# Kernel tuning notes

Hardware: AMD Instinct MI355X
Metric: run time of the kernel (lower is better)

## Reference

```python
import jax, jax.numpy as jnp
import numpy as np

EMBED = 1024
NUM_EXPERTS = 8
TOP_K = 2


def setup_inputs() -> dict:
    key = jax.random.key(0)
    ks = jax.random.split(key, 6)
    scale = EMBED ** -0.5  # keep activations numerically sane
    return {
        "x": jax.random.normal(ks[0], (4, 4096, EMBED), jnp.float32),
        "router_w": jax.random.normal(ks[1], (EMBED, NUM_EXPERTS), jnp.float32) * scale,
        "router_b": jnp.zeros((NUM_EXPERTS,), jnp.float32),
        "we_gate": jax.random.normal(ks[2], (NUM_EXPERTS, EMBED, EMBED), jnp.float32) * scale,
        "we_up": jax.random.normal(ks[3], (NUM_EXPERTS, EMBED, EMBED), jnp.float32) * scale,
        "we_down": jax.random.normal(ks[4], (NUM_EXPERTS, EMBED, EMBED), jnp.float32) * scale,
    }


def reference(x, router_w, router_b, we_gate, we_up, we_down):
    x_shape = x.shape
    x_flat = x.reshape(-1, x_shape[-1])            # [T, D]
    num_tokens = x_flat.shape[0]

    router_logits = x_flat @ router_w + router_b    # [T, E]
    topk_weights, topk_indices = jax.lax.top_k(router_logits, k=TOP_K)
    topk_weights = jax.nn.softmax(topk_weights, axis=-1)  # [T, K]

    token_idx_mesh = jnp.repeat(jnp.arange(num_tokens), TOP_K)  # [T*K]
    expert_idx_mesh = topk_indices.reshape(-1)                  # [T*K]

    sort_permutation = jnp.argsort(expert_idx_mesh)  # stable sort by expert
    sorted_expert_idx = expert_idx_mesh[sort_permutation]
    sorted_token_idx = token_idx_mesh[sort_permutation]
    group_sizes = jnp.bincount(sorted_expert_idx, length=NUM_EXPERTS)

    sorted_tokens = x_flat[sorted_token_idx]  # [T*K, D] gather (ragged dispatch)

    ff_gate = jax.lax.ragged_dot(sorted_tokens, we_gate, group_sizes)  # [T*K, D]
    ff_up = jax.lax.ragged_dot(sorted_tokens, we_up, group_sizes)      # [T*K, D]
    activated = jax.nn.silu(ff_gate) * ff_up
    ff_out = jax.lax.ragged_dot(activated, we_down, group_sizes)       # [T*K, D]

    # fuse router weighting into the combine (scatter-add) step
    sorted_weights = topk_weights.reshape(-1)[sort_permutation]  # [T*K]
    ff_out = ff_out * sorted_weights[:, None]

    output_flat = jnp.zeros_like(x_flat).at[sorted_token_idx].add(ff_out)
    return output_flat.reshape(x_shape)
```

## Files before the change

### kernel.cpp

```cpp
#include <hip/hip_runtime.h>
#include <hip/hip_bf16.h>
#include <cstdint>
#include <cstddef>

typedef unsigned short u16;
typedef unsigned int u32;
typedef __attribute__((ext_vector_type(8))) short short8;
typedef __attribute__((ext_vector_type(4))) float floatx4;

#define DD 1024
#define NE 8

#define GLOAD_LDS16(G, L)                                               \
  __builtin_amdgcn_global_load_lds(                                     \
      (const __attribute__((address_space(1))) void*)(G),               \
      (__attribute__((address_space(3))) void*)(L), 16, 0, 0)

__device__ __forceinline__ u16 f2bf(float f) {
  union { __hip_bfloat16 h; u16 u; } cv;
  cv.h = __float2bfloat16(f);
  return cv.u;
}

__device__ __forceinline__ float2 bf2f2(u32 u) {
  union { u32 v; float f; } lo, hi;
  lo.v = u << 16; hi.v = u & 0xffff0000u;
  float2 r; r.x = lo.f; r.y = hi.f; return r;
}

__global__ __launch_bounds__(256) void router_kernel(
    const float* __restrict__ x, const float* __restrict__ rw,
    const float* __restrict__ rb, int2* __restrict__ experts,
    float2* __restrict__ wts, u16* __restrict__ xbf, int T) {
  const int wave = threadIdx.x >> 6;
  const int lane = threadIdx.x & 63;
  const int t = blockIdx.x * 4 + wave;
  if (t >= T) return;
  const float* xr = x + (size_t)t * DD;
  float acc[NE] = {0.f, 0.f, 0.f, 0.f, 0.f, 0.f, 0.f, 0.f};
#pragma unroll
  for (int i = 0; i < 16; i++) {
    const int idx = lane + i * 64;
    const float xv = xr[idx];
    xbf[(size_t)t * DD + idx] = f2bf(xv);
    const float4* r4 = (const float4*)(rw + (size_t)idx * NE);
    float4 a = r4[0], b = r4[1];
    acc[0] += xv * a.x; acc[1] += xv * a.y; acc[2] += xv * a.z; acc[3] += xv * a.w;
    acc[4] += xv * b.x; acc[5] += xv * b.y; acc[6] += xv * b.z; acc[7] += xv * b.w;
  }
#pragma unroll
  for (int s = 1; s < 64; s <<= 1)
#pragma unroll
    for (int e = 0; e < NE; e++)
      acc[e] += __shfl_xor(acc[e], s);
  if (lane == 0) {
    float lg[NE];
#pragma unroll
    for (int e = 0; e < NE; e++) lg[e] = acc[e] + rb[e];
    float l0 = lg[0]; int i0 = 0;
#pragma unroll
    for (int e = 1; e < NE; e++) if (lg[e] > l0) { l0 = lg[e]; i0 = e; }
    float l1 = -3.4e38f; int i1 = 0;
#pragma unroll
    for (int e = 0; e < NE; e++) {
      if (e == i0) continue;
      if (lg[e] > l1) { l1 = lg[e]; i1 = e; }
    }
    const float w0 = 1.f / (1.f + expf(l1 - l0));
    experts[t] = make_int2(i0, i1);
    wts[t] = make_float2(w0, 1.f - w0);
  }
}

__global__ __launch_bounds__(256) void count_kernel(
    const int2* __restrict__ experts, int* __restrict__ counts, int T) {
  __shared__ int lc[NE];
  if (threadIdx.x < NE) lc[threadIdx.x] = 0;
  __syncthreads();
  const int t = blockIdx.x * 256 + threadIdx.x;
  if (t < T) {
    int2 e = experts[t];
    atomicAdd(&lc[e.x], 1);
    atomicAdd(&lc[e.y], 1);
  }
  __syncthreads();
  if (threadIdx.x < NE && lc[threadIdx.x] > 0)
    atomicAdd(&counts[threadIdx.x], lc[threadIdx.x]);
}

__global__ void offsets_kernel(const int* __restrict__ counts, int* __restrict__ offsets) {
  int s = 0;
  for (int e = 0; e < NE; e++) { offsets[e] = s; s += counts[e]; }
}

__global__ __launch_bounds__(256) void scatter_kernel(
    const int2* __restrict__ experts, const int* __restrict__ offsets,
    int* __restrict__ cursors, int* __restrict__ tok_id,
    int2* __restrict__ slots, int T) {
  __shared__ int lc[NE], lb[NE];
  if (threadIdx.x < NE) lc[threadIdx.x] = 0;
  __syncthreads();
  const int t = blockIdx.x * 256 + threadIdx.x;
  int2 e = make_int2(0, 0);
  int p0 = 0, p1 = 0;
  if (t < T) {
    e = experts[t];
    p0 = atomicAdd(&lc[e.x], 1);
    p1 = atomicAdd(&lc[e.y], 1);
  }
  __syncthreads();
  if (threadIdx.x < NE) lb[threadIdx.x] = atomicAdd(&cursors[threadIdx.x], lc[threadIdx.x]);
  __syncthreads();
  if (t < T) {
    const int s0 = offsets[e.x] + lb[e.x] + p0;
    const int s1 = offsets[e.y] + lb[e.y] + p1;
    tok_id[s0] = t;
    tok_id[s1] = t;
    slots[t] = make_int2(s0, s1);
  }
}

__global__ __launch_bounds__(256) void convert_kernel(
    const float* __restrict__ wg, const float* __restrict__ wu,
    const float* __restrict__ wd, u16* __restrict__ Wgu, u16* __restrict__ Wd) {
  const int z = blockIdx.z;
  const int mat = z >> 3;
  const int e = z & 7;
  const float* src = (mat == 0 ? wg : (mat == 1 ? wu : wd)) + (size_t)e * DD * DD;
  __shared__ float tile[64][65];
  const int k0 = blockIdx.y * 64, n0 = blockIdx.x * 64;
  const int tx = threadIdx.x & 63, ty = threadIdx.x >> 6;
#pragma unroll
  for (int i = 0; i < 16; i++) {
    const int kk = i * 4 + ty;
    tile[kk][tx] = src[(size_t)(k0 + kk) * DD + n0 + tx];
  }
  __syncthreads();
#pragma unroll
  for (int i = 0; i < 16; i++) {
    const int nn = i * 4 + ty;
    const int n = n0 + nn;
    const u16 h = f2bf(tile[tx][nn]);
    if (mat == 2) {
      Wd[((size_t)e * DD + n) * DD + k0 + tx] = h;
    } else {
      const int nc = ((n >> 3) << 4) | (mat << 3) | (n & 7);
      Wgu[((size_t)e * 2048 + nc) * DD + k0 + tx] = h;
    }
  }
}

__global__ __launch_bounds__(256) void gateup_kernel(
    const u16* __restrict__ xbf, const u16* __restrict__ Wgu,
    const int* __restrict__ tok_id, const int* __restrict__ offsets,
    const int* __restrict__ counts, u16* __restrict__ H) {
  const int e = blockIdx.z;
  const int cnt = counts[e];
  const int m0 = blockIdx.y * 128;
  if (m0 >= cnt) return;
  const int off = offsets[e];
  const int n0 = blockIdx.x * 128;

  __shared__ u16 As[128 * 64];
  __shared__ u16 Bs[128 * 64];

  const int t = threadIdx.x;
  const int lane = t & 63;
  const int wave = t >> 6;
  const int wm = (wave >> 1) * 64;
  const int wn = (wave & 1) * 64;
  const int r16 = lane & 15;
  const int quad = lane >> 4;

  const int drow = t >> 3;
  const int dpos = t & 7;
  const u16* srcA[4];
  const u16* srcB[4];
  const u16* bbase = Wgu + ((size_t)e * 2048 + n0) * DD;
#pragma unroll
  for (int i = 0; i < 4; i++) {
    const int row = drow + i * 32;
    int r = m0 + row; if (r > cnt - 1) r = cnt - 1;
    const int tok = tok_id[off + r];
    const int ka = (dpos ^ (row & 7)) * 8;
    srcA[i] = xbf + (size_t)tok * DD + ka;
    srcB[i] = bbase + (size_t)row * DD + ka;
  }

  floatx4 acc[4][4];
#pragma unroll
  for (int i = 0; i < 4; i++)
#pragma unroll
    for (int j = 0; j < 4; j++)
      acc[i][j] = (floatx4){0.f, 0.f, 0.f, 0.f};

#pragma unroll 1
  for (int k0 = 0; k0 < DD; k0 += 64) {
    __syncthreads();
#pragma unroll
    for (int i = 0; i < 4; i++) {
      GLOAD_LDS16(srcA[i] + k0, &As[t * 8 + i * 2048]);
      GLOAD_LDS16(srcB[i] + k0, &Bs[t * 8 + i * 2048]);
    }
    __syncthreads();
#pragma unroll
    for (int s = 0; s < 2; s++) {
      short8 a[4], b[4];
#pragma unroll
      for (int i = 0; i < 4; i++)
        a[i] = *(const short8*)&As[(wm + i * 16 + r16) * 64 + (((s << 2) + quad) ^ (r16 & 7)) * 8];
#pragma unroll
      for (int j = 0; j < 4; j++)
        b[j] = *(const short8*)&Bs[(wn + j * 16 + r16) * 64 + (((s << 2) + quad) ^ (r16 & 7)) * 8];
#pragma unroll
      for (int i = 0; i < 4; i++)
#pragma unroll
        for (int j = 0; j < 4; j++)
          acc[i][j] = __builtin_amdgcn_mfma_f32_16x16x32_bf16(a[i], b[j], acc[i][j], 0, 0, 0);
    }
  }

#pragma unroll
  for (int i = 0; i < 4; i++) {
    const int mb = m0 + wm + i * 16 + quad * 4;
#pragma unroll
    for (int j = 0; j < 4; j++) {
      const int nc = n0 + wn + j * 16 + r16;
      const int ng = ((nc >> 4) << 3) | (nc & 7);
#pragma unroll
      for (int r = 0; r < 4; r++) {
        const float v = acc[i][j][r];
        const float pv = __shfl_xor(v, 8);
        const float g = (lane & 8) ? pv : v;
        const float u = (lane & 8) ? v : pv;
        const float hv = g * u / (1.f + __expf(-g));
        const int m = mb + r;
        if (!(lane & 8) && m < cnt)
          H[(size_t)(off + m) * DD + ng] = f2bf(hv);
      }
    }
  }
}

__global__ __launch_bounds__(256) void down_kernel(
    const u16* __restrict__ H, const u16* __restrict__ Wd,
    const int* __restrict__ counts, const int* __restrict__ offsets,
    u16* __restrict__ Y, int TK2) {
  const int e = blockIdx.z;
  const int cnt = counts[e];
  const int m0 = blockIdx.y * 128;
  if (m0 >= cnt) return;
  const int off = offsets[e];
  const int n0 = blockIdx.x * 128;

  __shared__ u16 As[128 * 64];
  __shared__ u16 Bs[128 * 64];

  const int t = threadIdx.x;
  const int lane = t & 63;
  const int wave = t >> 6;
  const int wm = (wave >> 1) * 64;
  const int wn = (wave & 1) * 64;
  const int r16 = lane & 15;
  const int quad = lane >> 4;

  const int drow = t >> 3;
  const int dpos = t & 7;
  const u16* srcA[4];
  const u16* srcB[4];
  const u16* bbase = Wd + ((size_t)e * DD + n0) * DD;
#pragma unroll
  for (int i = 0; i < 4; i++) {
    const int row = drow + i * 32;
    int r = off + m0 + row; if (r > TK2 - 1) r = TK2 - 1;
    const int ka = (dpos ^ (row & 7)) * 8;
    srcA[i] = H + (size_t)r * DD + ka;
    srcB[i] = bbase + (size_t)row * DD + ka;
  }

  floatx4 acc[4][4];
#pragma unroll
  for (int i = 0; i < 4; i++)
#pragma unroll
    for (int j = 0; j < 4; j++)
      acc[i][j] = (floatx4){0.f, 0.f, 0.f, 0.f};

#pragma unroll 1
  for (int k0 = 0; k0 < DD; k0 += 64) {
    __syncthreads();
#pragma unroll
    for (int i = 0; i < 4; i++) {
      GLOAD_LDS16(srcA[i] + k0, &As[t * 8 + i * 2048]);
      GLOAD_LDS16(srcB[i] + k0, &Bs[t * 8 + i * 2048]);
    }
    __syncthreads();
#pragma unroll
    for (int s = 0; s < 2; s++) {
      short8 a[4], b[4];
#pragma unroll
      for (int i = 0; i < 4; i++)
        a[i] = *(const short8*)&As[(wm + i * 16 + r16) * 64 + (((s << 2) + quad) ^ (r16 & 7)) * 8];
#pragma unroll
      for (int j = 0; j < 4; j++)
        b[j] = *(const short8*)&Bs[(wn + j * 16 + r16) * 64 + (((s << 2) + quad) ^ (r16 & 7)) * 8];
#pragma unroll
      for (int i = 0; i < 4; i++)
#pragma unroll
        for (int j = 0; j < 4; j++)
          acc[i][j] = __builtin_amdgcn_mfma_f32_16x16x32_bf16(a[i], b[j], acc[i][j], 0, 0, 0);
    }
  }

#pragma unroll
  for (int i = 0; i < 4; i++) {
    const int mb = m0 + wm + i * 16 + quad * 4;
#pragma unroll
    for (int r = 0; r < 4; r++) {
      const int m = mb + r;
      if (m < cnt) {
        u16* yrow = Y + (size_t)(off + m) * DD + n0 + wn + r16;
#pragma unroll
        for (int j = 0; j < 4; j++)
          yrow[j * 16] = f2bf(acc[i][j][r]);
      }
    }
  }
}

__global__ __launch_bounds__(256) void combine_kernel(
    const u16* __restrict__ Y, const int2* __restrict__ slots,
    const float2* __restrict__ wts, float* __restrict__ out, int T) {
  const int wave = threadIdx.x >> 6;
  const int lane = threadIdx.x & 63;
  const int t = blockIdx.x * 4 + wave;
  if (t >= T) return;
  const int2 s = slots[t];
  const float2 w = wts[t];
  const uint4* y0 = (const uint4*)(Y + (size_t)s.x * DD);
  const uint4* y1 = (const uint4*)(Y + (size_t)s.y * DD);
  float4* o = (float4*)(out + (size_t)t * DD);
#pragma unroll
  for (int c = 0; c < 2; c++) {
    const int idx = lane + c * 64;
    const uint4 a = y0[idx];
    const uint4 b = y1[idx];
    const u32 au[4] = {a.x, a.y, a.z, a.w};
    const u32 bu[4] = {b.x, b.y, b.z, b.w};
    float4 r[2];
#pragma unroll
    for (int q = 0; q < 4; q++) {
      const float2 fa = bf2f2(au[q]);
      const float2 fb = bf2f2(bu[q]);
      ((float*)r)[q * 2]     = w.x * fa.x + w.y * fb.x;
      ((float*)r)[q * 2 + 1] = w.x * fa.y + w.y * fb.y;
    }
    o[idx * 2]     = r[0];
    o[idx * 2 + 1] = r[1];
  }
}

extern "C" void kernel_launch(void* const* d_in, const int* in_sizes, int n_in,
                              void* d_out, int out_size, void* d_ws, size_t ws_size,
                              hipStream_t stream) {
  const float* x  = (const float*)d_in[0];
  const float* rw = (const float*)d_in[1];
  const float* rb = (const float*)d_in[2];
  const float* wg = (const float*)d_in[3];
  const float* wu = (const float*)d_in[4];
  const float* wd = (const float*)d_in[5];
  float* out = (float*)d_out;
  const int T = in_sizes[0] / DD;
  const int TK2 = 2 * T;

  char* p = (char*)d_ws;
  int* ctrl = (int*)p; p += 256;
  int2* experts = (int2*)p;  p += (size_t)T * 8;
  float2* wtsp  = (float2*)p; p += (size_t)T * 8;
  int* tok_id   = (int*)p;   p += (size_t)TK2 * 4;
  int2* slots   = (int2*)p;  p += (size_t)T * 8;
  u16* Wd       = (u16*)p;   p += (size_t)NE * DD * DD * 2;
  u16* H        = (u16*)p;   p += (size_t)TK2 * DD * 2;
  u16* Wgu      = (u16*)p;
  u16* xbf      = (u16*)(p + (size_t)NE * 2048 * DD * 2);
  u16* Y        = (u16*)p;
  p += (size_t)TK2 * DD * 2;
  if ((size_t)(p - (char*)d_ws) > ws_size) return;

  hipMemsetAsync(ctrl, 0, 256, stream);

  router_kernel<<<T / 4, 256, 0, stream>>>(x, rw, rb, experts, wtsp, xbf, T);
  count_kernel<<<T / 256, 256, 0, stream>>>(experts, ctrl, T);
  offsets_kernel<<<1, 1, 0, stream>>>(ctrl, ctrl + 16);
  scatter_kernel<<<T / 256, 256, 0, stream>>>(experts, ctrl + 16, ctrl + 8, tok_id, slots, T);
  convert_kernel<<<dim3(16, 16, 24), 256, 0, stream>>>(wg, wu, wd, Wgu, Wd);
  gateup_kernel<<<dim3(16, (T + 127) / 128, NE), 256, 0, stream>>>(
      xbf, Wgu, tok_id, ctrl + 16, ctrl, H);
  down_kernel<<<dim3(8, (T + 127) / 128, NE), 256, 0, stream>>>(
      H, Wd, ctrl, ctrl + 16, Y, TK2);
  combine_kernel<<<T / 4, 256, 0, stream>>>(Y, slots, wtsp, out, T);
}
```

Before: 509.0 us.

## Use 32x32 MFMA in expert GEMMs and fold counting into router

The gate/up and down expert GEMMs switch from 16x16x32 to 32x32x16 bf16 MFMA tiles, with 2x2 16-wide accumulators per wave instead of 4x4 4-wide ones, so fewer LDS fragment loads are issued per MFMA. Expert counting moves into the router kernel through shared-memory atomics, and the scatter kernel computes offsets inline, which removes the separate count launch. The offsets kernel now runs after scatter. The epilogue row/column mapping is reworked for the 32x32 output layout, and the gate/up interleave shuffle by 8 lanes is kept, which is a correctness risk if the column pairing differs under the new layout.

```diff
diff --git a/kernel.cpp b/kernel.cpp
--- a/kernel.cpp
+++ b/kernel.cpp
@@ -6,7 +6,7 @@
 typedef unsigned short u16;
 typedef unsigned int u32;
 typedef __attribute__((ext_vector_type(8))) short short8;
-typedef __attribute__((ext_vector_type(4))) float floatx4;
+typedef __attribute__((ext_vector_type(16))) float floatx16;
 
 #define DD 1024
 #define NE 8
@@ -31,70 +31,59 @@
 __global__ __launch_bounds__(256) void router_kernel(
     const float* __restrict__ x, const float* __restrict__ rw,
     const float* __restrict__ rb, int2* __restrict__ experts,
-    float2* __restrict__ wts, u16* __restrict__ xbf, int T) {
+    float2* __restrict__ wts, u16* __restrict__ xbf,
+    int* __restrict__ counts, int T) {
+  __shared__ int lc[NE];
+  if (threadIdx.x < NE) lc[threadIdx.x] = 0;
+  __syncthreads();
   const int wave = threadIdx.x >> 6;
   const int lane = threadIdx.x & 63;
   const int t = blockIdx.x * 4 + wave;
-  if (t >= T) return;
-  const float* xr = x + (size_t)t * DD;
-  float acc[NE] = {0.f, 0.f, 0.f, 0.f, 0.f, 0.f, 0.f, 0.f};
-#pragma unroll
-  for (int i = 0; i < 16; i++) {
-    const int idx = lane + i * 64;
-    const float xv = xr[idx];
-    xbf[(size_t)t * DD + idx] = f2bf(xv);
-    const float4* r4 = (const float4*)(rw + (size_t)idx * NE);
-    float4 a = r4[0], b = r4[1];
-    acc[0] += xv * a.x; acc[1] += xv * a.y; acc[2] += xv * a.z; acc[3] += xv * a.w;
-    acc[4] += xv * b.x; acc[5] += xv * b.y; acc[6] += xv * b.z; acc[7] += xv * b.w;
-  }
-#pragma unroll
-  for (int s = 1; s < 64; s <<= 1)
-#pragma unroll
-    for (int e = 0; e < NE; e++)
-      acc[e] += __shfl_xor(acc[e], s);
-  if (lane == 0) {
-    float lg[NE];
-#pragma unroll
-    for (int e = 0; e < NE; e++) lg[e] = acc[e] + rb[e];
-    float l0 = lg[0]; int i0 = 0;
-#pragma unroll
-    for (int e = 1; e < NE; e++) if (lg[e] > l0) { l0 = lg[e]; i0 = e; }
-    float l1 = -3.4e38f; int i1 = 0;
-#pragma unroll
-    for (int e = 0; e < NE; e++) {
-      if (e == i0) continue;
-      if (lg[e] > l1) { l1 = lg[e]; i1 = e; }
-    }
-    const float w0 = 1.f / (1.f + expf(l1 - l0));
-    experts[t] = make_int2(i0, i1);
-    wts[t] = make_float2(w0, 1.f - w0);
-  }
-}
-
-__global__ __launch_bounds__(256) void count_kernel(
-    const int2* __restrict__ experts, int* __restrict__ counts, int T) {
-  __shared__ int lc[NE];
-  if (threadIdx.x < NE) lc[threadIdx.x] = 0;
-  __syncthreads();
-  const int t = blockIdx.x * 256 + threadIdx.x;
   if (t < T) {
-    int2 e = experts[t];
-    atomicAdd(&lc[e.x], 1);
-    atomicAdd(&lc[e.y], 1);
+    const float* xr = x + (size_t)t * DD;
+    float acc[NE] = {0.f, 0.f, 0.f, 0.f, 0.f, 0.f, 0.f, 0.f};
+#pragma unroll
+    for (int i = 0; i < 16; i++) {
+      const int idx = lane + i * 64;
+      const float xv = xr[idx];
+      xbf[(size_t)t * DD + idx] = f2bf(xv);
+      const float4* r4 = (const float4*)(rw + (size_t)idx * NE);
+      float4 a = r4[0], b = r4[1];
+      acc[0] += xv * a.x; acc[1] += xv * a.y; acc[2] += xv * a.z; acc[3] += xv * a.w;
+      acc[4] += xv * b.x; acc[5] += xv * b.y; acc[6] += xv * b.z; acc[7] += xv * b.w;
+    }
+#pragma unroll
+    for (int s = 1; s < 64; s <<= 1)
+#pragma unroll
+      for (int e = 0; e < NE; e++)
+        acc[e] += __shfl_xor(acc[e], s);
+    if (lane == 0) {
+      float lg[NE];
+#pragma unroll
+      for (int e = 0; e < NE; e++) lg[e] = acc[e] + rb[e];
+      float l0 = lg[0]; int i0 = 0;
+#pragma unroll
+      for (int e = 1; e < NE; e++) if (lg[e] > l0) { l0 = lg[e]; i0 = e; }
+      float l1 = -3.4e38f; int i1 = 0;
+#pragma unroll
+      for (int e = 0; e < NE; e++) {
+        if (e == i0) continue;
+        if (lg[e] > l1) { l1 = lg[e]; i1 = e; }
+      }
+      const float w0 = 1.f / (1.f + expf(l1 - l0));
+      experts[t] = make_int2(i0, i1);
+      wts[t] = make_float2(w0, 1.f - w0);
+      atomicAdd(&lc[i0], 1);
+      atomicAdd(&lc[i1], 1);
+    }
   }
   __syncthreads();
   if (threadIdx.x < NE && lc[threadIdx.x] > 0)
     atomicAdd(&counts[threadIdx.x], lc[threadIdx.x]);
 }
 
-__global__ void offsets_kernel(const int* __restrict__ counts, int* __restrict__ offsets) {
-  int s = 0;
-  for (int e = 0; e < NE; e++) { offsets[e] = s; s += counts[e]; }
-}
-
 __global__ __launch_bounds__(256) void scatter_kernel(
-    const int2* __restrict__ experts, const int* __restrict__ offsets,
+    const int2* __restrict__ experts, const int* __restrict__ counts,
     int* __restrict__ cursors, int* __restrict__ tok_id,
     int2* __restrict__ slots, int T) {
   __shared__ int lc[NE], lb[NE];
@@ -112,12 +101,21 @@
   if (threadIdx.x < NE) lb[threadIdx.x] = atomicAdd(&cursors[threadIdx.x], lc[threadIdx.x]);
   __syncthreads();
   if (t < T) {
-    const int s0 = offsets[e.x] + lb[e.x] + p0;
-    const int s1 = offsets[e.y] + lb[e.y] + p1;
+    int offs[NE];
+    int s = 0;
+#pragma unroll
+    for (int i = 0; i < NE; i++) { offs[i] = s; s += counts[i]; }
+    const int s0 = offs[e.x] + lb[e.x] + p0;
+    const int s1 = offs[e.y] + lb[e.y] + p1;
     tok_id[s0] = t;
     tok_id[s1] = t;
     slots[t] = make_int2(s0, s1);
   }
+}
+
+__global__ void offsets_kernel(const int* __restrict__ counts, int* __restrict__ offsets) {
+  int s = 0;
+  for (int e = 0; e < NE; e++) { offsets[e] = s; s += counts[e]; }
 }
 
 __global__ __launch_bounds__(256) void convert_kernel(
@@ -169,8 +167,8 @@
   const int wave = t >> 6;
   const int wm = (wave >> 1) * 64;
   const int wn = (wave & 1) * 64;
-  const int r16 = lane & 15;
-  const int quad = lane >> 4;
+  const int r32 = lane & 31;
+  const int half = lane >> 5;
 
   const int drow = t >> 3;
   const int dpos = t & 7;
@@ -187,12 +185,12 @@
     srcB[i] = bbase + (size_t)row * DD + ka;
   }
 
-  floatx4 acc[4][4];
-#pragma unroll
-  for (int i = 0; i < 4; i++)
-#pragma unroll
-    for (int j = 0; j < 4; j++)
-      acc[i][j] = (floatx4){0.f, 0.f, 0.f, 0.f};
+  floatx16 acc[2][2];
+#pragma unroll
+  for (int i = 0; i < 2; i++)
+#pragma unroll
+    for (int j = 0; j < 2; j++)
+      acc[i][j] = (floatx16)(0.f);
 
 #pragma unroll 1
   for (int k0 = 0; k0 < DD; k0 += 64) {
@@ -204,37 +202,37 @@
     }
     __syncthreads();
 #pragma unroll
-    for (int s = 0; s < 2; s++) {
-      short8 a[4], b[4];
-#pragma unroll
-      for (int i = 0; i < 4; i++)
-        a[i] = *(const short8*)&As[(wm + i * 16 + r16) * 64 + (((s << 2) + quad) ^ (r16 & 7)) * 8];
-#pragma unroll
-      for (int j = 0; j < 4; j++)
-        b[j] = *(const short8*)&Bs[(wn + j * 16 + r16) * 64 + (((s << 2) + quad) ^ (r16 & 7)) * 8];
-#pragma unroll
-      for (int i = 0; i < 4; i++)
-#pragma unroll
-        for (int j = 0; j < 4; j++)
-          acc[i][j] = __builtin_amdgcn_mfma_f32_16x16x32_bf16(a[i], b[j], acc[i][j], 0, 0, 0);
-    }
-  }
-
-#pragma unroll
-  for (int i = 0; i < 4; i++) {
-    const int mb = m0 + wm + i * 16 + quad * 4;
-#pragma unroll
-    for (int j = 0; j < 4; j++) {
-      const int nc = n0 + wn + j * 16 + r16;
+    for (int s = 0; s < 4; s++) {
+      const int kc = ((2 * s + half) ^ (r32 & 7)) * 8;
+      short8 a[2], b[2];
+#pragma unroll
+      for (int i = 0; i < 2; i++)
+        a[i] = *(const short8*)&As[(wm + i * 32 + r32) * 64 + kc];
+#pragma unroll
+      for (int j = 0; j < 2; j++)
+        b[j] = *(const short8*)&Bs[(wn + j * 32 + r32) * 64 + kc];
+#pragma unroll
+      for (int i = 0; i < 2; i++)
+#pragma unroll
+        for (int j = 0; j < 2; j++)
+          acc[i][j] = __builtin_amdgcn_mfma_f32_32x32x16_bf16(a[i], b[j], acc[i][j], 0, 0, 0);
+    }
+  }
+
+#pragma unroll
+  for (int i = 0; i < 2; i++) {
+#pragma unroll
+    for (int j = 0; j < 2; j++) {
+      const int nc = n0 + wn + j * 32 + r32;
       const int ng = ((nc >> 4) << 3) | (nc & 7);
 #pragma unroll
-      for (int r = 0; r < 4; r++) {
-        const float v = acc[i][j][r];
+      for (int reg = 0; reg < 16; reg++) {
+        const float v = acc[i][j][reg];
         const float pv = __shfl_xor(v, 8);
         const float g = (lane & 8) ? pv : v;
         const float u = (lane & 8) ? v : pv;
         const float hv = g * u / (1.f + __expf(-g));
-        const int m = mb + r;
+        const int m = m0 + wm + i * 32 + (reg & 3) + 8 * (reg >> 2) + 4 * half;
         if (!(lane & 8) && m < cnt)
           H[(size_t)(off + m) * DD + ng] = f2bf(hv);
       }
@@ -261,8 +259,8 @@
   const int wave = t >> 6;
   const int wm = (wave >> 1) * 64;
   const int wn = (wave & 1) * 64;
-  const int r16 = lane & 15;
-  const int quad = lane >> 4;
+  const int r32 = lane & 31;
+  const int half = lane >> 5;
 
   const int drow = t >> 3;
   const int dpos = t & 7;
@@ -278,12 +276,12 @@
     srcB[i] = bbase + (size_t)row * DD + ka;
   }
 
-  floatx4 acc[4][4];
-#pragma unroll
-  for (int i = 0; i < 4; i++)
-#pragma unroll
-    for (int j = 0; j < 4; j++)
-      acc[i][j] = (floatx4){0.f, 0.f, 0.f, 0.f};
+  floatx16 acc[2][2];
+#pragma unroll
+  for (int i = 0; i < 2; i++)
+#pragma unroll
+    for (int j = 0; j < 2; j++)
+      acc[i][j] = (floatx16)(0.f);
 
 #pragma unroll 1
   for (int k0 = 0; k0 < DD; k0 += 64) {
@@ -295,33 +293,33 @@
     }
     __syncthreads();
 #pragma unroll
-    for (int s = 0; s < 2; s++) {
-      short8 a[4], b[4];
-#pragma unroll
-      for (int i = 0; i < 4; i++)
-        a[i] = *(const short8*)&As[(wm + i * 16 + r16) * 64 + (((s << 2) + quad) ^ (r16 & 7)) * 8];
-#pragma unroll
-      for (int j = 0; j < 4; j++)
-        b[j] = *(const short8*)&Bs[(wn + j * 16 + r16) * 64 + (((s << 2) + quad) ^ (r16 & 7)) * 8];
-#pragma unroll
-      for (int i = 0; i < 4; i++)
-#pragma unroll
-        for (int j = 0; j < 4; j++)
-          acc[i][j] = __builtin_amdgcn_mfma_f32_16x16x32_bf16(a[i], b[j], acc[i][j], 0, 0, 0);
-    }
-  }
-
-#pragma unroll
-  for (int i = 0; i < 4; i++) {
-    const int mb = m0 + wm + i * 16 + quad * 4;
-#pragma unroll
-    for (int r = 0; r < 4; r++) {
-      const int m = mb + r;
+    for (int s = 0; s < 4; s++) {
+      const int kc = ((2 * s + half) ^ (r32 & 7)) * 8;
+      short8 a[2], b[2];
+#pragma unroll
+      for (int i = 0; i < 2; i++)
+        a[i] = *(const short8*)&As[(wm + i * 32 + r32) * 64 + kc];
+#pragma unroll
+      for (int j = 0; j < 2; j++)
+        b[j] = *(const short8*)&Bs[(wn + j * 32 + r32) * 64 + kc];
+#pragma unroll
+      for (int i = 0; i < 2; i++)
+#pragma unroll
+        for (int j = 0; j < 2; j++)
+          acc[i][j] = __builtin_amdgcn_mfma_f32_32x32x16_bf16(a[i], b[j], acc[i][j], 0, 0, 0);
+    }
+  }
+
+#pragma unroll
+  for (int i = 0; i < 2; i++) {
+#pragma unroll
+    for (int reg = 0; reg < 16; reg++) {
+      const int m = m0 + wm + i * 32 + (reg & 3) + 8 * (reg >> 2) + 4 * half;
       if (m < cnt) {
-        u16* yrow = Y + (size_t)(off + m) * DD + n0 + wn + r16;
-#pragma unroll
-        for (int j = 0; j < 4; j++)
-          yrow[j * 16] = f2bf(acc[i][j][r]);
+        u16* yrow = Y + (size_t)(off + m) * DD + n0 + wn + r32;
+#pragma unroll
+        for (int j = 0; j < 2; j++)
+          yrow[j * 32] = f2bf(acc[i][j][reg]);
       }
     }
   }
@@ -388,10 +386,9 @@
 
   hipMemsetAsync(ctrl, 0, 256, stream);
 
-  router_kernel<<<T / 4, 256, 0, stream>>>(x, rw, rb, experts, wtsp, xbf, T);
-  count_kernel<<<T / 256, 256, 0, stream>>>(experts, ctrl, T);
+  router_kernel<<<T / 4, 256, 0, stream>>>(x, rw, rb, experts, wtsp, xbf, ctrl, T);
+  scatter_kernel<<<T / 256, 256, 0, stream>>>(experts, ctrl, ctrl + 8, tok_id, slots, T);
   offsets_kernel<<<1, 1, 0, stream>>>(ctrl, ctrl + 16);
-  scatter_kernel<<<T / 256, 256, 0, stream>>>(experts, ctrl + 16, ctrl + 8, tok_id, slots, T);
   convert_kernel<<<dim3(16, 16, 24), 256, 0, stream>>>(wg, wu, wd, Wgu, Wd);
   gateup_kernel<<<dim3(16, (T + 127) / 128, NE), 256, 0, stream>>>(
       xbf, Wgu, tok_id, ctrl + 16, ctrl, H);
```

Measured after the change: 529.6 us. 4.0% more time.
